# Kernel tuning notes

Measured on AMD Instinct MI355X. Metric: run time of the kernel, lower is better.

Reference implementation:

```python
import jax, jax.numpy as jnp
from jax import lax
import numpy as np

B, N, C = 16, 4096, 64
RATIO = 0.25
M = int(N * RATIO)      # 1024 sampled centers
R = 0.2                 # radius
K = 64                  # max_num_neighbors
H = 128                 # MLP hidden/out width
NEG = -1e30


def setup_inputs() -> dict:
    key = jax.random.key(0)
    k1, k2, k3, k4 = jax.random.split(key, 4)
    pos = jax.random.uniform(k1, (B, N, 3), dtype=jnp.float32)
    x = jax.random.normal(k2, (B, N, C), dtype=jnp.float32)
    W1 = jax.random.normal(k3, (C + 3, H), dtype=jnp.float32) / np.sqrt(C + 3)
    b1 = jnp.zeros((H,), jnp.float32)
    W2 = jax.random.normal(k4, (H, H), dtype=jnp.float32) / np.sqrt(H)
    b2 = jnp.zeros((H,), jnp.float32)
    return {"x": x, "pos": pos, "W1": W1, "b1": b1, "W2": W2, "b2": b2}


def _fps_single(p, m):
    """Farthest point sampling on one cloud p:[N,3] -> m int32 indices (start at 0)."""
    n = p.shape[0]
    big = jnp.full((n,), jnp.finfo(p.dtype).max, dtype=p.dtype)

    def step(carry, _):
        dists, last = carry
        d = jnp.sum((p - p[last]) ** 2, axis=-1)       # [N]
        dists = jnp.minimum(dists, d)
        nxt = jnp.argmax(dists).astype(jnp.int32)
        return (dists, nxt), nxt

    (_, _), idxs = lax.scan(step, (big, jnp.int32(0)), None, length=m - 1)
    return jnp.concatenate([jnp.zeros((1,), jnp.int32), idxs])


def reference(x, pos, W1, b1, W2, b2):
    # --- FPS: sample M centers per cloud ---
    idx = jax.vmap(lambda p: _fps_single(p, M))(pos)                 # [B,M] int32
    pos_s = jax.vmap(lambda p, i: p[i])(pos, idx)                    # [B,M,3]

    # --- radius ball query: pairwise sq-dists via |a|^2+|b|^2-2ab (no [B,M,N,3]) ---
    pn = jnp.sum(pos * pos, axis=-1)                                 # [B,N]
    sn = jnp.sum(pos_s * pos_s, axis=-1)                             # [B,M]
    d2 = sn[:, :, None] + pn[:, None, :] - 2.0 * jnp.einsum("bmc,bnc->bmn", pos_s, pos)
    mask = d2 <= R * R                                               # [B,M,N]

    # first K in-radius neighbors by index (torch_cluster-style capped neighbor list)
    ar = jnp.arange(N, dtype=jnp.int32)
    scored = jnp.where(mask, -ar[None, None, :], -N)                 # valid -> -idx
    vals, _ = lax.top_k(scored, K)                                   # [B,M,K]
    nbr = -vals                                                      # neighbor indices, N = invalid
    valid = nbr < N                                                  # [B,M,K]
    nbr_c = jnp.minimum(nbr, N - 1)

    # --- gather -> MLP -> masked max aggregation (PointConv, aggr='max') ---
    x_j = jax.vmap(lambda xb, ib: xb[ib])(x, nbr_c)                  # [B,M,K,C]
    pos_j = jax.vmap(lambda pb, ib: pb[ib])(pos, nbr_c)              # [B,M,K,3]
    feat = jnp.concatenate([x_j, pos_j - pos_s[:, :, None, :]], axis=-1)  # [B,M,K,C+3]

    h = jax.nn.relu(jnp.einsum("bmkc,ch->bmkh", feat, W1) + b1)
    h = jax.nn.relu(jnp.einsum("bmkh,hg->bmkg", h, W2) + b2)          # [B,M,K,H]

    h = jnp.where(valid[..., None], h, NEG)
    out = jnp.max(h, axis=2)                                          # [B,M,H]
    out = jnp.where(jnp.any(valid, axis=2)[..., None], out, 0.0)
    return out, pos_s
```

## Files before the change

### kernel.cpp

```cpp
#include <hip/hip_runtime.h>
#include <cstdint>
#include <cstddef>

#define BB 16
#define NN 4096
#define CC 64
#define MM 1024
#define KK 64
#define HH 128
#define NEGV -1.0e30f

#define FTH 256
#define FPT 16
#define NPROD 16
#define GTOT 256
#define PSTRIDE 32

#define KC1 96
#define SA 104
#define SH 136
#define HSTRIDE 41984

typedef __attribute__((ext_vector_type(8))) short bf16x8;
typedef __attribute__((ext_vector_type(4))) float f32x4;
typedef __attribute__((ext_vector_type(2))) float f32x2;

__device__ __forceinline__ unsigned int f2bf(float f) {
  unsigned int u = __float_as_uint(f);
  return (u + 0x7fffu + ((u >> 16) & 1u)) >> 16;
}
__device__ __forceinline__ void split2(float f, unsigned int& h, unsigned int& l) {
  h = f2bf(f);
  float hf = __uint_as_float(h << 16);
  l = f2bf(f - hf);
}

template <int CTRL, int RM>
__device__ __forceinline__ void dpp_max64(unsigned int& hi, unsigned int& lo) {
  unsigned int shi = (unsigned int)__builtin_amdgcn_update_dpp(
      (int)hi, (int)hi, CTRL, RM, 0xf, false);
  unsigned int slo = (unsigned int)__builtin_amdgcn_update_dpp(
      (int)lo, (int)lo, CTRL, RM, 0xf, false);
  unsigned long long cur = ((unsigned long long)hi << 32) | lo;
  unsigned long long oth = ((unsigned long long)shi << 32) | slo;
  if (oth > cur) { hi = shi; lo = slo; }
}

__global__ __launch_bounds__(256) void pn_kernel(const float* __restrict__ pos,
                                                 float* __restrict__ pn) {
#pragma clang fp contract(off)
  int i = blockIdx.x * 256 + threadIdx.x;
  if (i < BB * NN) {
    float x = pos[(size_t)i * 3 + 0];
    float y = pos[(size_t)i * 3 + 1];
    float z = pos[(size_t)i * 3 + 2];
    pn[i] = (x * x + y * y) + z * z;
  }
}

__global__ __launch_bounds__(128) void wprep_kernel(
    const float* __restrict__ W1, const float* __restrict__ W2,
    unsigned short* __restrict__ W1Th, unsigned short* __restrict__ W1Tl,
    unsigned short* __restrict__ W2Th, unsigned short* __restrict__ W2Tl) {
  const int n = blockIdx.x, t = threadIdx.x;
  if (t < KC1) {
    float v = (t < 67) ? W1[(size_t)t * HH + n] : 0.0f;
    unsigned int h, l; split2(v, h, l);
    W1Th[n * KC1 + t] = (unsigned short)h;
    W1Tl[n * KC1 + t] = (unsigned short)l;
  }
  {
    float v = W2[(size_t)t * HH + n];
    unsigned int h, l; split2(v, h, l);
    W2Th[n * HH + t] = (unsigned short)h;
    W2Tl[n * HH + t] = (unsigned short)l;
  }
}

__global__ void init_kernel(unsigned int* progress, unsigned int* claim) {
  int t = threadIdx.x;
  if (t < NPROD * PSTRIDE) progress[t] = 0u;
  if (t == NPROD * PSTRIDE) *claim = 0u;
}

__global__ __launch_bounds__(512, 2) void fused_kernel(
    const float* __restrict__ pos, const float* __restrict__ x,
    const float* __restrict__ pn,
    float* __restrict__ pos_s_ws, float* __restrict__ pos_s_out,
    const unsigned short* __restrict__ W1Th, const unsigned short* __restrict__ W1Tl,
    const unsigned short* __restrict__ W2Th, const unsigned short* __restrict__ W2Tl,
    const float* __restrict__ b1, const float* __restrict__ b2,
    float* __restrict__ out,
    unsigned int* __restrict__ progress, unsigned int* __restrict__ claim) {
#pragma clang fp contract(off)
  __shared__ __attribute__((aligned(16))) unsigned char LBUF[83968];
  const int t = threadIdx.x;
  const int lane = t & 63;

  if (blockIdx.x < NPROD) {
    if (t >= FTH) return;
    __builtin_amdgcn_s_setprio(3);
    const int wv = t >> 6;
    const int b = blockIdx.x;
    float4* P4 = (float4*)LBUF;
    float* SXa = (float*)(LBUF + 65536);
    float* SYa = (float*)(LBUF + 69632);
    float* SZa = (float*)(LBUF + 73728);
    unsigned long long* cand = (unsigned long long*)(LBUF + 77824);
    const float* pb = pos + (size_t)b * NN * 3;
    f32x2 px[8], py[8], pz[8], dd[8];
#pragma unroll
    for (int j = 0; j < FPT; ++j) {
      int i = t + j * FTH;
      float xx = pb[i * 3 + 0], yy = pb[i * 3 + 1], zz = pb[i * 3 + 2];
      P4[i] = make_float4(xx, yy, zz, 0.0f);
      px[j >> 1][j & 1] = xx;
      py[j >> 1][j & 1] = yy;
      pz[j >> 1][j & 1] = zz;
      dd[j >> 1][j & 1] = 3.4028234663852886e38f;
    }
    __syncthreads();
    float4 c4 = P4[0];
    float sx = c4.x, sy = c4.y, sz = c4.z;
    if (t == 0) { SXa[0] = sx; SYa[0] = sy; SZa[0] = sz; }

    for (int m = 1; m < MM; ++m) {
      float bv = -1.0f;
      int   bi = 0;
      f32x2 s2x = {sx, sx}, s2y = {sy, sy}, s2z = {sz, sz};
#pragma unroll
      for (int k = 0; k < 8; ++k) {
        f32x2 dx = px[k] - s2x, dy = py[k] - s2y, dz = pz[k] - s2z;
        f32x2 d2 = (dx * dx + dy * dy) + dz * dz;
        float n0 = fminf(dd[k][0], d2[0]);
        float n1 = fminf(dd[k][1], d2[1]);
        dd[k][0] = n0;
        dd[k][1] = n1;
        if (n0 > bv) { bv = n0; bi = t + ((2 * k) << 8); }
        if (n1 > bv) { bv = n1; bi = t + ((2 * k + 1) << 8); }
      }
      unsigned int kh = __float_as_uint(bv);
      unsigned int kl = ~(unsigned int)bi;
      dpp_max64<0x111, 0xf>(kh, kl);
      dpp_max64<0x112, 0xf>(kh, kl);
      dpp_max64<0x114, 0xf>(kh, kl);
      dpp_max64<0x118, 0xf>(kh, kl);
      dpp_max64<0x142, 0xa>(kh, kl);
      dpp_max64<0x143, 0xc>(kh, kl);
      if (lane == 63)
        cand[(m & 1) * 4 + wv] = ((unsigned long long)kh << 32) | kl;
      __syncthreads();
      unsigned long long best = cand[(m & 1) * 4 + 0];
#pragma unroll
      for (int w = 1; w < 4; ++w) {
        unsigned long long ok = cand[(m & 1) * 4 + w];
        best = ok > best ? ok : best;
      }
      int fi = (int)(~(unsigned int)(best & 0xffffffffull));
      float4 w4 = P4[fi];
      sx = w4.x; sy = w4.y; sz = w4.z;
      if (t == 0) {
        SXa[m] = sx; SYa[m] = sy; SZa[m] = sz;
        if ((m & 15) == 15) {
          int base = m - 15;
          for (int j = 0; j < 16; ++j) {
            size_t o = ((size_t)b * MM + base + j) * 3;
            __hip_atomic_store(&pos_s_ws[o + 0], SXa[base + j], __ATOMIC_RELAXED, __HIP_MEMORY_SCOPE_AGENT);
            __hip_atomic_store(&pos_s_ws[o + 1], SYa[base + j], __ATOMIC_RELAXED, __HIP_MEMORY_SCOPE_AGENT);
            __hip_atomic_store(&pos_s_ws[o + 2], SZa[base + j], __ATOMIC_RELAXED, __HIP_MEMORY_SCOPE_AGENT);
          }
        } else if ((m & 15) == 0) {
          asm volatile("s_waitcnt vmcnt(0)" ::: "memory");
          __hip_atomic_store(&progress[b * PSTRIDE], (unsigned int)m,
                             __ATOMIC_RELAXED, __HIP_MEMORY_SCOPE_AGENT);
        }
      }
    }
    __syncthreads();
    if (t == 0) {
      asm volatile("s_waitcnt vmcnt(0)" ::: "memory");
      __hip_atomic_store(&progress[b * PSTRIDE], (unsigned int)MM,
                         __ATOMIC_RELAXED, __HIP_MEMORY_SCOPE_AGENT);
    }
    for (int i = t; i < MM; i += FTH) {
      size_t o = ((size_t)b * MM + i) * 3;
      pos_s_out[o + 0] = SXa[i];
      pos_s_out[o + 1] = SYa[i];
      pos_s_out[o + 2] = SZa[i];
    }
    return;
  }

  const int h = t >> 8;
  const int th = t & 255;
  const int wvh = (t >> 6) & 3;
  unsigned char* HB = LBUF + h * HSTRIDE;
  unsigned short* Ah = (unsigned short*)HB;
  unsigned short* Al = (unsigned short*)(HB + 64 * SA * 2);
  unsigned short* Hh = (unsigned short*)HB;
  unsigned short* Hl = (unsigned short*)(HB + 64 * SH * 2);
  int* nbr_s = (int*)(HB + 34816);
  unsigned long long* masksL = (unsigned long long*)(HB + 35072);
  int* prefixL = (int*)(HB + 35584);
  float* ctr = (float*)(HB + 35840);
  int* cntS = (int*)(HB + 35856);
  volatile int* cidShare = (int*)(LBUF + 83960);
  const int r = lane & 15, q = lane >> 4;
  const int wbase = wvh * 32;

  while (true) {
    if (t == 0) {
      unsigned int i = __hip_atomic_fetch_add(claim, 2u, __ATOMIC_RELAXED,
                                              __HIP_MEMORY_SCOPE_AGENT);
      *cidShare = (int)i;
    }
    __syncthreads();
    int i0 = *cidShare;
    if (i0 >= BB * MM) break;
    const int i = i0 + h;
    const bool active = (i < BB * MM);
    const int cid = active ? (((i & 15) << 10) | (i >> 4)) : 0;
    const int b = cid >> 10;
    const int m = cid & 1023;

    if (active && th < 64) {
      while ((int)__hip_atomic_load(&progress[b * PSTRIDE], __ATOMIC_RELAXED,
                                    __HIP_MEMORY_SCOPE_AGENT) <= m)
        __builtin_amdgcn_s_sleep(64);
    }
    if (active && th < 3)
      ctr[th] = __hip_atomic_load(&pos_s_ws[(size_t)cid * 3 + th],
                                  __ATOMIC_RELAXED, __HIP_MEMORY_SCOPE_AGENT);
    __syncthreads();

    const float sx = ctr[0], sy = ctr[1], sz = ctr[2];
    const float sn = (sx * sx + sy * sy) + sz * sz;
    const float* pb = pos + (size_t)b * NN * 3;
    const float* pnb = pn + (size_t)b * NN;
    if (active) {
#pragma unroll
      for (int cc = 0; cc < 16; ++cc) {
        int c = (wvh << 4) + cc;
        int n = (c << 6) + lane;
        float xx = pb[n * 3 + 0], yy = pb[n * 3 + 1], zz = pb[n * 3 + 2];
        float dot = __builtin_fmaf(sz, zz, __builtin_fmaf(sy, yy, sx * xx));
        float d2 = (sn + pnb[n]) - 2.0f * dot;
        bool pred = d2 <= 0.04f;
        unsigned long long mask = __ballot(pred);
        if (lane == 0) masksL[c] = mask;
      }
    }
    __syncthreads();
    if (active && th < 64) {
      int pc = (int)__popcll(masksL[lane]);
      int incl = pc;
#pragma unroll
      for (int off = 1; off < 64; off <<= 1) {
        int o2 = __shfl_up(incl, off, 64);
        if (lane >= off) incl += o2;
      }
      prefixL[lane] = incl - pc;
      if (lane == 63) *cntS = incl < KK ? incl : KK;
    }
    __syncthreads();
    const int cnt = *cntS;
    if (active) {
#pragma unroll
      for (int cc = 0; cc < 16; ++cc) {
        int c = (wvh << 4) + cc;
        unsigned long long mk = masksL[c];
        bool pred = (mk >> lane) & 1ull;
        int slot = prefixL[c] + (int)__popcll(mk & ((1ull << lane) - 1ull));
        if (pred && slot < KK) nbr_s[slot] = (c << 6) + lane;
      }
    }
    __syncthreads();

    if (active) {
      const int kn = th >> 2, p = th & 3;
      float vals[16];
      float d0 = 0.0f, d1 = 0.0f, d2v = 0.0f;
      if (kn < cnt) {
        int n = nbr_s[kn];
        const float* xp = x + ((size_t)b * NN + n) * CC + p * 16;
#pragma unroll
        for (int ii = 0; ii < 4; ++ii) {
          float4 v = ((const float4*)xp)[ii];
          vals[ii * 4 + 0] = v.x; vals[ii * 4 + 1] = v.y;
          vals[ii * 4 + 2] = v.z; vals[ii * 4 + 3] = v.w;
        }
        if (p == 0) {
          const float* pp = pos + ((size_t)b * NN + n) * 3;
          d0 = pp[0] - sx; d1 = pp[1] - sy; d2v = pp[2] - sz;
        }
      } else {
#pragma unroll
        for (int ii = 0; ii < 16; ++ii) vals[ii] = 0.0f;
      }
#pragma unroll
      for (int j = 0; j < 16; j += 2) {
        unsigned int h0, l0, h1, l1;
        split2(vals[j], h0, l0);
        split2(vals[j + 1], h1, l1);
        int c = p * 16 + j;
        *(unsigned int*)&Ah[kn * SA + c] = h0 | (h1 << 16);
        *(unsigned int*)&Al[kn * SA + c] = l0 | (l1 << 16);
      }
      if (p == 0) {
        unsigned int h0, l0, h1, l1, h2, l2;
        split2(d0, h0, l0); split2(d1, h1, l1); split2(d2v, h2, l2);
        *(unsigned int*)&Ah[kn * SA + 64] = h0 | (h1 << 16);
        *(unsigned int*)&Al[kn * SA + 64] = l0 | (l1 << 16);
        *(unsigned int*)&Ah[kn * SA + 66] = h2;
        *(unsigned int*)&Al[kn * SA + 66] = l2;
      } else if (p == 1) {
#pragma unroll
        for (int c = 68; c < 80; c += 2) {
          *(unsigned int*)&Ah[kn * SA + c] = 0u;
          *(unsigned int*)&Al[kn * SA + c] = 0u;
        }
      } else if (p == 2) {
#pragma unroll
        for (int c = 80; c < 96; c += 2) {
          *(unsigned int*)&Ah[kn * SA + c] = 0u;
          *(unsigned int*)&Al[kn * SA + c] = 0u;
        }
      }
    }
    __syncthreads();

    f32x4 acc[4][2];
#pragma unroll
    for (int mt = 0; mt < 4; ++mt)
#pragma unroll
      for (int nt = 0; nt < 2; ++nt) acc[mt][nt] = (f32x4)0.0f;

    if (active) {
#pragma unroll
      for (int kc = 0; kc < 3; ++kc) {
        bf16x8 bh[2], bl[2];
#pragma unroll
        for (int nt = 0; nt < 2; ++nt) {
          int o = (wbase + nt * 16 + r) * KC1 + kc * 32 + q * 8;
          bh[nt] = *(const bf16x8*)(W1Th + o);
          bl[nt] = *(const bf16x8*)(W1Tl + o);
        }
#pragma unroll
        for (int mt = 0; mt < 4; ++mt) {
          int o = (mt * 16 + r) * SA + kc * 32 + q * 8;
          bf16x8 ah = *(const bf16x8*)&Ah[o];
          bf16x8 al = *(const bf16x8*)&Al[o];
#pragma unroll
          for (int nt = 0; nt < 2; ++nt) {
            acc[mt][nt] = __builtin_amdgcn_mfma_f32_16x16x32_bf16(ah, bh[nt], acc[mt][nt], 0, 0, 0);
            acc[mt][nt] = __builtin_amdgcn_mfma_f32_16x16x32_bf16(al, bh[nt], acc[mt][nt], 0, 0, 0);
            acc[mt][nt] = __builtin_amdgcn_mfma_f32_16x16x32_bf16(ah, bl[nt], acc[mt][nt], 0, 0, 0);
          }
        }
      }
    }
    __syncthreads();

    if (active) {
      float b1v[2] = { b1[wbase + r], b1[wbase + 16 + r] };
#pragma unroll
      for (int mt = 0; mt < 4; ++mt)
#pragma unroll
        for (int nt = 0; nt < 2; ++nt)
#pragma unroll
          for (int ii = 0; ii < 4; ++ii) {
            int mm = mt * 16 + q * 4 + ii;
            int n = wbase + nt * 16 + r;
            float v = fmaxf(acc[mt][nt][ii] + b1v[nt], 0.0f);
            unsigned int hh2, ll2; split2(v, hh2, ll2);
            Hh[mm * SH + n] = (unsigned short)hh2;
            Hl[mm * SH + n] = (unsigned short)ll2;
          }
    }
    __syncthreads();

#pragma unroll
    for (int mt = 0; mt < 4; ++mt)
#pragma unroll
      for (int nt = 0; nt < 2; ++nt) acc[mt][nt] = (f32x4)0.0f;
    if (active) {
#pragma unroll
      for (int kc = 0; kc < 4; ++kc) {
        bf16x8 bh[2], bl[2];
#pragma unroll
        for (int nt = 0; nt < 2; ++nt) {
          int o = (wbase + nt * 16 + r) * HH + kc * 32 + q * 8;
          bh[nt] = *(const bf16x8*)(W2Th + o);
          bl[nt] = *(const bf16x8*)(W2Tl + o);
        }
#pragma unroll
        for (int mt = 0; mt < 4; ++mt) {
          int o = (mt * 16 + r) * SH + kc * 32 + q * 8;
          bf16x8 ah = *(const bf16x8*)&Hh[o];
          bf16x8 al = *(const bf16x8*)&Hl[o];
#pragma unroll
          for (int nt = 0; nt < 2; ++nt) {
            acc[mt][nt] = __builtin_amdgcn_mfma_f32_16x16x32_bf16(ah, bh[nt], acc[mt][nt], 0, 0, 0);
            acc[mt][nt] = __builtin_amdgcn_mfma_f32_16x16x32_bf16(al, bh[nt], acc[mt][nt], 0, 0, 0);
            acc[mt][nt] = __builtin_amdgcn_mfma_f32_16x16x32_bf16(ah, bl[nt], acc[mt][nt], 0, 0, 0);
          }
        }
      }
      float b2v[2] = { b2[wbase + r], b2[wbase + 16 + r] };
#pragma unroll
      for (int nt = 0; nt < 2; ++nt) {
        float vmax = NEGV;
#pragma unroll
        for (int mt = 0; mt < 4; ++mt)
#pragma unroll
          for (int ii = 0; ii < 4; ++ii) {
            int mm = mt * 16 + q * 4 + ii;
            float v = fmaxf(acc[mt][nt][ii] + b2v[nt], 0.0f);
            if (mm < cnt) vmax = fmaxf(vmax, v);
          }
        vmax = fmaxf(vmax, __shfl_xor(vmax, 16, 64));
        vmax = fmaxf(vmax, __shfl_xor(vmax, 32, 64));
        if (q == 0)
          out[(size_t)cid * HH + wbase + nt * 16 + r] = (cnt > 0) ? vmax : 0.0f;
      }
    }
    __syncthreads();
  }
}

extern "C" void kernel_launch(void* const* d_in, const int* in_sizes, int n_in,
                              void* d_out, int out_size, void* d_ws, size_t ws_size,
                              hipStream_t stream) {
  const float* x   = (const float*)d_in[0];
  const float* pos = (const float*)d_in[1];
  const float* W1  = (const float*)d_in[2];
  const float* b1  = (const float*)d_in[3];
  const float* W2  = (const float*)d_in[4];
  const float* b2  = (const float*)d_in[5];
  float* out = (float*)d_out;
  float* pos_s_out = out + (size_t)BB * MM * HH;

  char* ws = (char*)d_ws;
  float* pos_s_ws = (float*)(ws);
  float* pn       = (float*)(ws + 196608);
  unsigned short* W1Th = (unsigned short*)(ws + 458752);
  unsigned short* W1Tl = (unsigned short*)(ws + 483328);
  unsigned short* W2Th = (unsigned short*)(ws + 507904);
  unsigned short* W2Tl = (unsigned short*)(ws + 540672);
  unsigned int* progress = (unsigned int*)(ws + 573440);
  unsigned int* claim    = (unsigned int*)(ws + 575488);

  wprep_kernel<<<HH, 128, 0, stream>>>(W1, W2, W1Th, W1Tl, W2Th, W2Tl);
  pn_kernel<<<(BB * NN) / 256, 256, 0, stream>>>(pos, pn);
  init_kernel<<<1, NPROD * PSTRIDE + 64, 0, stream>>>(progress, claim);
  fused_kernel<<<GTOT, 512, 0, stream>>>(pos, x, pn, pos_s_ws, pos_s_out,
                                         W1Th, W1Tl, W2Th, W2Tl, b1, b2, out,
                                         progress, claim);
}
```

Measured before the change: 799.2 us.

## Merge prep kernels, tree-reduce FPS argmax, parallelize center publishing

Drops the pn and init kernels. The per-point squared norm is now computed inline in the ball query, and zeroing of the progress and claim counters moves into wprep_kernel, which cuts two launches. The FPS per-thread argmax becomes a pairwise tree reduction instead of a serial compare chain, which shortens the critical path of the serial FPS loop. The batched store of sampled centers to the workspace is spread over 16 threads instead of one thread looping. Tie-breaking in the tree reduction still favors the lower index, which should keep results identical.

```diff
diff --git a/kernel.cpp b/kernel.cpp
--- a/kernel.cpp
+++ b/kernel.cpp
@@ -46,23 +46,16 @@
   if (oth > cur) { hi = shi; lo = slo; }
 }
 
-__global__ __launch_bounds__(256) void pn_kernel(const float* __restrict__ pos,
-                                                 float* __restrict__ pn) {
-#pragma clang fp contract(off)
-  int i = blockIdx.x * 256 + threadIdx.x;
-  if (i < BB * NN) {
-    float x = pos[(size_t)i * 3 + 0];
-    float y = pos[(size_t)i * 3 + 1];
-    float z = pos[(size_t)i * 3 + 2];
-    pn[i] = (x * x + y * y) + z * z;
-  }
-}
-
 __global__ __launch_bounds__(128) void wprep_kernel(
     const float* __restrict__ W1, const float* __restrict__ W2,
     unsigned short* __restrict__ W1Th, unsigned short* __restrict__ W1Tl,
-    unsigned short* __restrict__ W2Th, unsigned short* __restrict__ W2Tl) {
+    unsigned short* __restrict__ W2Th, unsigned short* __restrict__ W2Tl,
+    unsigned int* __restrict__ progress, unsigned int* __restrict__ claim) {
   const int n = blockIdx.x, t = threadIdx.x;
+  if (n == 0) {
+    for (int j = t; j < NPROD * PSTRIDE; j += 128) progress[j] = 0u;
+    if (t == 0) *claim = 0u;
+  }
   if (t < KC1) {
     float v = (t < 67) ? W1[(size_t)t * HH + n] : 0.0f;
     unsigned int h, l; split2(v, h, l);
@@ -77,15 +70,8 @@
   }
 }
 
-__global__ void init_kernel(unsigned int* progress, unsigned int* claim) {
-  int t = threadIdx.x;
-  if (t < NPROD * PSTRIDE) progress[t] = 0u;
-  if (t == NPROD * PSTRIDE) *claim = 0u;
-}
-
 __global__ __launch_bounds__(512, 2) void fused_kernel(
     const float* __restrict__ pos, const float* __restrict__ x,
-    const float* __restrict__ pn,
     float* __restrict__ pos_s_ws, float* __restrict__ pos_s_out,
     const unsigned short* __restrict__ W1Th, const unsigned short* __restrict__ W1Tl,
     const unsigned short* __restrict__ W2Th, const unsigned short* __restrict__ W2Tl,
@@ -125,9 +111,8 @@
     if (t == 0) { SXa[0] = sx; SYa[0] = sy; SZa[0] = sz; }
 
     for (int m = 1; m < MM; ++m) {
-      float bv = -1.0f;
-      int   bi = 0;
       f32x2 s2x = {sx, sx}, s2y = {sy, sy}, s2z = {sz, sz};
+      float nv[16];
 #pragma unroll
       for (int k = 0; k < 8; ++k) {
         f32x2 dx = px[k] - s2x, dy = py[k] - s2y, dz = pz[k] - s2z;
@@ -136,9 +121,35 @@
         float n1 = fminf(dd[k][1], d2[1]);
         dd[k][0] = n0;
         dd[k][1] = n1;
-        if (n0 > bv) { bv = n0; bi = t + ((2 * k) << 8); }
-        if (n1 > bv) { bv = n1; bi = t + ((2 * k + 1) << 8); }
-      }
+        nv[2 * k] = n0;
+        nv[2 * k + 1] = n1;
+      }
+      float tv[8]; int ti[8];
+#pragma unroll
+      for (int k = 0; k < 8; ++k) {
+        bool c = nv[2 * k + 1] > nv[2 * k];
+        tv[k] = c ? nv[2 * k + 1] : nv[2 * k];
+        ti[k] = c ? (2 * k + 1) : (2 * k);
+      }
+      float uv[4]; int ui[4];
+#pragma unroll
+      for (int k = 0; k < 4; ++k) {
+        bool c = tv[2 * k + 1] > tv[2 * k];
+        uv[k] = c ? tv[2 * k + 1] : tv[2 * k];
+        ui[k] = c ? ti[2 * k + 1] : ti[2 * k];
+      }
+      float wv2[2]; int wi2[2];
+#pragma unroll
+      for (int k = 0; k < 2; ++k) {
+        bool c = uv[2 * k + 1] > uv[2 * k];
+        wv2[k] = c ? uv[2 * k + 1] : uv[2 * k];
+        wi2[k] = c ? ui[2 * k + 1] : ui[2 * k];
+      }
+      bool cf = wv2[1] > wv2[0];
+      float bv = cf ? wv2[1] : wv2[0];
+      int bj = cf ? wi2[1] : wi2[0];
+      int bi = t + (bj << 8);
+
       unsigned int kh = __float_as_uint(bv);
       unsigned int kl = ~(unsigned int)bi;
       dpp_max64<0x111, 0xf>(kh, kl);
@@ -159,21 +170,20 @@
       int fi = (int)(~(unsigned int)(best & 0xffffffffull));
       float4 w4 = P4[fi];
       sx = w4.x; sy = w4.y; sz = w4.z;
-      if (t == 0) {
-        SXa[m] = sx; SYa[m] = sy; SZa[m] = sz;
-        if ((m & 15) == 15) {
-          int base = m - 15;
-          for (int j = 0; j < 16; ++j) {
-            size_t o = ((size_t)b * MM + base + j) * 3;
-            __hip_atomic_store(&pos_s_ws[o + 0], SXa[base + j], __ATOMIC_RELAXED, __HIP_MEMORY_SCOPE_AGENT);
-            __hip_atomic_store(&pos_s_ws[o + 1], SYa[base + j], __ATOMIC_RELAXED, __HIP_MEMORY_SCOPE_AGENT);
-            __hip_atomic_store(&pos_s_ws[o + 2], SZa[base + j], __ATOMIC_RELAXED, __HIP_MEMORY_SCOPE_AGENT);
-          }
-        } else if ((m & 15) == 0) {
-          asm volatile("s_waitcnt vmcnt(0)" ::: "memory");
-          __hip_atomic_store(&progress[b * PSTRIDE], (unsigned int)m,
-                             __ATOMIC_RELAXED, __HIP_MEMORY_SCOPE_AGENT);
-        }
+      if (t == 0) { SXa[m] = sx; SYa[m] = sy; SZa[m] = sz; }
+      if ((m & 15) == 15) {
+        if (t < 16) {
+          int idx = (m - 15) + t;
+          float fx = SXa[idx], fy = SYa[idx], fz = SZa[idx];
+          size_t o = ((size_t)b * MM + idx) * 3;
+          __hip_atomic_store(&pos_s_ws[o + 0], fx, __ATOMIC_RELAXED, __HIP_MEMORY_SCOPE_AGENT);
+          __hip_atomic_store(&pos_s_ws[o + 1], fy, __ATOMIC_RELAXED, __HIP_MEMORY_SCOPE_AGENT);
+          __hip_atomic_store(&pos_s_ws[o + 2], fz, __ATOMIC_RELAXED, __HIP_MEMORY_SCOPE_AGENT);
+        }
+      } else if ((m & 15) == 0 && t == 0) {
+        asm volatile("s_waitcnt vmcnt(0)" ::: "memory");
+        __hip_atomic_store(&progress[b * PSTRIDE], (unsigned int)m,
+                           __ATOMIC_RELAXED, __HIP_MEMORY_SCOPE_AGENT);
       }
     }
     __syncthreads();
@@ -236,15 +246,15 @@
     const float sx = ctr[0], sy = ctr[1], sz = ctr[2];
     const float sn = (sx * sx + sy * sy) + sz * sz;
     const float* pb = pos + (size_t)b * NN * 3;
-    const float* pnb = pn + (size_t)b * NN;
     if (active) {
 #pragma unroll
       for (int cc = 0; cc < 16; ++cc) {
         int c = (wvh << 4) + cc;
         int n = (c << 6) + lane;
         float xx = pb[n * 3 + 0], yy = pb[n * 3 + 1], zz = pb[n * 3 + 2];
+        float pnn = (xx * xx + yy * yy) + zz * zz;
         float dot = __builtin_fmaf(sz, zz, __builtin_fmaf(sy, yy, sx * xx));
-        float d2 = (sn + pnb[n]) - 2.0f * dot;
+        float d2 = (sn + pnn) - 2.0f * dot;
         bool pred = d2 <= 0.04f;
         unsigned long long mask = __ballot(pred);
         if (lane == 0) masksL[c] = mask;
@@ -442,7 +452,6 @@
 
   char* ws = (char*)d_ws;
   float* pos_s_ws = (float*)(ws);
-  float* pn       = (float*)(ws + 196608);
   unsigned short* W1Th = (unsigned short*)(ws + 458752);
   unsigned short* W1Tl = (unsigned short*)(ws + 483328);
   unsigned short* W2Th = (unsigned short*)(ws + 507904);
@@ -450,10 +459,9 @@
   unsigned int* progress = (unsigned int*)(ws + 573440);
   unsigned int* claim    = (unsigned int*)(ws + 575488);
 
-  wprep_kernel<<<HH, 128, 0, stream>>>(W1, W2, W1Th, W1Tl, W2Th, W2Tl);
-  pn_kernel<<<(BB * NN) / 256, 256, 0, stream>>>(pos, pn);
-  init_kernel<<<1, NPROD * PSTRIDE + 64, 0, stream>>>(progress, claim);
-  fused_kernel<<<GTOT, 512, 0, stream>>>(pos, x, pn, pos_s_ws, pos_s_out,
+  wprep_kernel<<<HH, 128, 0, stream>>>(W1, W2, W1Th, W1Tl, W2Th, W2Tl,
+                                       progress, claim);
+  fused_kernel<<<GTOT, 512, 0, stream>>>(pos, x, pos_s_ws, pos_s_out,
                                          W1Th, W1Tl, W2Th, W2Tl, b1, b2, out,
                                          progress, claim);
 }
```

New measurement: 767.5 us. 1.04x faster.
